# Kernel optimization log

Hardware: AMD Instinct MI355X
Metric: run time of the kernel (lower is better)

The kernel has to match this reference:

```python
import jax, jax.numpy as jnp
import numpy as np

N, E = 50000, 800000
IN_F, HID_F, OUT_F = 128, 128, 32


def setup_inputs() -> dict:
    key = jax.random.key(0)
    ks = jax.random.split(key, 16)
    glorot = lambda k, i, o: jax.random.normal(k, (i, o), jnp.float32) * (2.0 / (i + o)) ** 0.5
    return {
        "x": jax.random.normal(ks[0], (N, IN_F), jnp.float32),
        "src": jax.random.randint(ks[1], (E,), 0, N, jnp.int64),
        "dst": jax.random.randint(ks[2], (E,), 0, N, jnp.int64),
        # layer 0: mean aggregator
        "W_self0": glorot(ks[3], IN_F, HID_F),
        "W_neigh0": glorot(ks[4], IN_F, HID_F),
        "b0": jnp.zeros((HID_F,), jnp.float32),
        # layers 1,2: gcn aggregator (fc_neigh only)
        "W_neigh1": glorot(ks[5], HID_F, HID_F),
        "b1": jnp.zeros((HID_F,), jnp.float32),
        "W_neigh2": glorot(ks[6], HID_F, HID_F),
        "b2": jnp.zeros((HID_F,), jnp.float32),
        # layer 3: mean aggregator
        "W_self3": glorot(ks[7], HID_F, OUT_F),
        "W_neigh3": glorot(ks[8], HID_F, OUT_F),
        "b3": jnp.zeros((OUT_F,), jnp.float32),
    }


def _l2_normalize(x, eps=1e-12):
    # torch F.normalize(x): x / max(||x||_2, eps) along dim 1
    n = jnp.sqrt(jnp.sum(x * x, axis=1, keepdims=True))
    return x / jnp.maximum(n, eps)


def _agg_sum(h, src, dst, n):
    # sum of in-neighbor (src) features onto dst nodes: [N, d]
    return jax.ops.segment_sum(h[src], dst, num_segments=n)


def _sage_mean(h, src, dst, deg, W_self, W_neigh, b):
    nbr = _agg_sum(h, src, dst, h.shape[0]) / jnp.maximum(deg, 1.0)[:, None]
    return h @ W_self + nbr @ W_neigh + b


def _sage_gcn(h, src, dst, deg, W_neigh, b):
    hn = (_agg_sum(h, src, dst, h.shape[0]) + h) / (deg + 1.0)[:, None]
    return hn @ W_neigh + b


def reference(x, src, dst, W_self0, W_neigh0, b0, W_neigh1, b1, W_neigh2, b2,
              W_self3, W_neigh3, b3):
    n = x.shape[0]
    deg = jax.ops.segment_sum(jnp.ones_like(dst, jnp.float32), dst, num_segments=n)
    h = _l2_normalize(x)
    h = jax.nn.relu(_sage_mean(h, src, dst, deg, W_self0, W_neigh0, b0))
    h = jax.nn.relu(_sage_gcn(h, src, dst, deg, W_neigh1, b1))
    h = jax.nn.relu(_sage_gcn(h, src, dst, deg, W_neigh2, b2))
    h = _sage_mean(h, src, dst, deg, W_self3, W_neigh3, b3)  # no relu on last layer
    return h
```

## Files before the change

### kernel.cpp

```cpp
#include <hip/hip_runtime.h>

#define NN 50000
#define NE 800000
#define F  128
#define FO 32

#define RSH  8
#define RSZ  256
#define NBKT 196
#define CAP  5120
#define PCHUNK 4096
#define NPB  ((NE + PCHUNK - 1) / PCHUNK)

typedef _Float16 h16;
typedef h16   half8 __attribute__((ext_vector_type(8)));
typedef h16   h16x2 __attribute__((ext_vector_type(2)));
typedef float f32x4 __attribute__((ext_vector_type(4)));

__global__ __launch_bounds__(256) void k_part(const int* __restrict__ src,
        const int* __restrict__ dst, int* __restrict__ bcur, int* __restrict__ barea) {
    __shared__ int cnt[NBKT];
    __shared__ int base[NBKT];
    const int tid = threadIdx.x;
    const int e0  = blockIdx.x * PCHUNK;
    for (int i = tid; i < NBKT; i += 256) cnt[i] = 0;
    __syncthreads();
    #pragma unroll
    for (int k = 0; k < PCHUNK / 256; ++k) {
        int e = e0 + k * 256 + tid;
        if (e < NE) atomicAdd(&cnt[dst[e] >> RSH], 1);
    }
    __syncthreads();
    for (int i = tid; i < NBKT; i += 256)
        base[i] = atomicAdd(&bcur[i], cnt[i]);
    __syncthreads();
    for (int i = tid; i < NBKT; i += 256) cnt[i] = base[i];
    __syncthreads();
    #pragma unroll
    for (int k = 0; k < PCHUNK / 256; ++k) {
        int e = e0 + k * 256 + tid;
        if (e < NE) {
            int d = dst[e], s = src[e];
            int b = d >> RSH;
            int p = atomicAdd(&cnt[b], 1);
            barea[b * CAP + p] = ((d & (RSZ - 1)) << 16) | s;
        }
    }
}

__global__ __launch_bounds__(256) void k_bscan(const int* __restrict__ bcur,
        int* __restrict__ bpre, int* __restrict__ offs) {
    __shared__ int ws[4];
    const int tid = threadIdx.x, lane = tid & 63, wv = tid >> 6;
    int v = (tid < NBKT) ? bcur[tid] : 0;
    int incl = v;
    #pragma unroll
    for (int d = 1; d < 64; d <<= 1) {
        int t = __shfl_up(incl, d, 64);
        if (lane >= d) incl += t;
    }
    if (lane == 63) ws[wv] = incl;
    __syncthreads();
    if (tid == 0) {
        int run = 0;
        #pragma unroll
        for (int w = 0; w < 4; ++w) { int t = ws[w]; ws[w] = run; run += t; }
    }
    __syncthreads();
    int excl = ws[wv] + incl - v;
    if (tid < NBKT) bpre[tid] = excl;
    if (tid == NBKT - 1) offs[NN] = excl + v;
}

__global__ __launch_bounds__(256) void k_bfill(const int* __restrict__ barea,
        const int* __restrict__ bcur, const int* __restrict__ bpre,
        int* __restrict__ offs, float* __restrict__ degf, int* __restrict__ csr) {
    __shared__ int hist_cur[RSZ];
    __shared__ int ws[4];
    const int r = blockIdx.x, tid = threadIdx.x;
    const int nb    = bcur[r];
    const int gbase = bpre[r];
    const int node  = (r << RSH) + tid;
    hist_cur[tid] = 0;
    __syncthreads();
    const int* area = barea + r * CAP;
    for (int i = tid; i < nb; i += 256) atomicAdd(&hist_cur[area[i] >> 16], 1);
    __syncthreads();
    const int v = hist_cur[tid];
    const int lane = tid & 63, wv = tid >> 6;
    int incl = v;
    #pragma unroll
    for (int d = 1; d < 64; d <<= 1) {
        int t = __shfl_up(incl, d, 64);
        if (lane >= d) incl += t;
    }
    if (lane == 63) ws[wv] = incl;
    __syncthreads();
    if (tid == 0) {
        int run = 0;
        #pragma unroll
        for (int w = 0; w < 4; ++w) { int t = ws[w]; ws[w] = run; run += t; }
    }
    __syncthreads();
    const int ex = ws[wv] + incl - v;
    if (node < NN) {
        offs[node] = gbase + ex;
        degf[node] = (float)v;
    }
    __syncthreads();
    hist_cur[tid] = gbase + ex;
    __syncthreads();
    for (int i = tid; i < nb; i += 256) {
        int pk = area[i];
        int p = atomicAdd(&hist_cur[pk >> 16], 1);
        csr[p] = pk & 0xFFFF;
    }
}

__device__ __forceinline__ void wprep_one(const float* __restrict__ W,
        h16* __restrict__ Wf, int idx, int NC, int NCT) {
    if (idx >= 128 * NC) return;
    int k = idx / NC, n = idx - k * NC;
    int kt = k >> 5, g = (k & 31) >> 3, j = k & 7;
    int ct = n >> 4;
    int lane = g * 16 + (n & 15);
    float w = W[idx];
    h16 hi = (h16)w;
    h16 lo = (h16)(w - (float)hi);
    int base = ((kt * NCT + ct) * 64 + lane) * 8 + j;
    Wf[base] = hi;
    Wf[base + NCT * 2048] = lo;
}

__global__ __launch_bounds__(256) void k_wprep_all(
        const float* __restrict__ S0, const float* __restrict__ N0,
        const float* __restrict__ N1, const float* __restrict__ N2,
        const float* __restrict__ S3, const float* __restrict__ N3,
        h16* fS0, h16* fN0, h16* fN1, h16* fN2, h16* fS3, h16* fN3) {
    int bb = blockIdx.x, tid = threadIdx.x;
    if (bb < 256) {
        const float* W = bb < 64 ? S0 : bb < 128 ? N0 : bb < 192 ? N1 : N2;
        h16*        Wf = bb < 64 ? fS0 : bb < 128 ? fN0 : bb < 192 ? fN1 : fN2;
        wprep_one(W, Wf, (bb & 63) * 256 + tid, 128, 8);
    } else {
        int b2 = bb - 256;
        const float* W = b2 < 16 ? S3 : N3;
        h16*        Wf = b2 < 16 ? fS3 : fN3;
        wprep_one(W, Wf, (b2 & 15) * 256 + tid, 32, 2);
    }
}

__global__ __launch_bounds__(256) void k_l2norm(const float* __restrict__ x,
        h16* __restrict__ hhi, h16* __restrict__ hlo) {
    const int wid  = (int)((blockIdx.x * 256 + threadIdx.x) >> 6);
    const int lane = threadIdx.x & 63;
    if (wid >= NN) return;
    const float2* xr = (const float2*)(x + (size_t)wid * F);
    float2 v = xr[lane];
    float ss = v.x * v.x + v.y * v.y;
    #pragma unroll
    for (int d = 1; d < 64; d <<= 1) ss += __shfl_xor(ss, d, 64);
    float inv = 1.0f / fmaxf(sqrtf(ss), 1e-12f);
    float ox = v.x * inv, oy = v.y * inv;
    h16 hx = (h16)ox, hy = (h16)oy;
    h16x2 vhi = {hx, hy};
    h16x2 vlo = {(h16)(ox - (float)hx), (h16)(oy - (float)hy)};
    *(h16x2*)(hhi + (size_t)wid * F + lane * 2) = vhi;
    *(h16x2*)(hlo + (size_t)wid * F + lane * 2) = vlo;
}

template<int NCT, bool OUT16>
__device__ __forceinline__ void mfma_cols(const half8* Ahi, const half8* Alo,
        const h16* __restrict__ Wf, void* __restrict__ out, int row0, int l) {
    const int cdc = l & 15;
    const int cdr = (l >> 4) * 4;
    #pragma unroll
    for (int ct = 0; ct < NCT; ++ct) {
        f32x4 acc = {0.f, 0.f, 0.f, 0.f};
        #pragma unroll
        for (int kt = 0; kt < 4; ++kt) {
            half8 bh = *(const half8*)(Wf + (size_t)(((kt * NCT + ct) * 64 + l) * 8));
            half8 bl = *(const half8*)(Wf + (size_t)((((4 + kt) * NCT + ct) * 64 + l) * 8));
            acc = __builtin_amdgcn_mfma_f32_16x16x32_f16(Ahi[kt], bh, acc, 0, 0, 0);
            acc = __builtin_amdgcn_mfma_f32_16x16x32_f16(Alo[kt], bh, acc, 0, 0, 0);
            acc = __builtin_amdgcn_mfma_f32_16x16x32_f16(Ahi[kt], bl, acc, 0, 0, 0);
        }
        #pragma unroll
        for (int r = 0; r < 4; ++r) {
            int gr = row0 + cdr + r;
            if (gr < NN) {
                size_t oi = (size_t)gr * (NCT * 16) + ct * 16 + cdc;
                if constexpr (OUT16) ((h16*)out)[oi] = (h16)acc[r];
                else                 ((float*)out)[oi] = acc[r];
            }
        }
    }
}

template<int NCTA, int NCTB, bool A16, bool B16>
__global__ __launch_bounds__(256) void k_mfma(const h16* __restrict__ hhi,
        const h16* __restrict__ hlo, const h16* __restrict__ WfA,
        const h16* __restrict__ WfB, void* __restrict__ outA,
        void* __restrict__ outB) {
    const int tid = threadIdx.x;
    const int l   = tid & 63;
    const int wv  = tid >> 6;
    const int row0 = blockIdx.x * 64 + wv * 16;
    int ar = row0 + (l & 15); if (ar >= NN) ar = NN - 1;
    const size_t ab = (size_t)ar * F + (l >> 4) * 8;
    half8 Ahi[4], Alo[4];
    #pragma unroll
    for (int kt = 0; kt < 4; ++kt) {
        Ahi[kt] = *(const half8*)(hhi + ab + kt * 32);
        Alo[kt] = *(const half8*)(hlo + ab + kt * 32);
    }
    mfma_cols<NCTA, A16>(Ahi, Alo, WfA, outA, row0, l);
    if constexpr (NCTB > 0) mfma_cols<NCTB, B16>(Ahi, Alo, WfB, outB, row0, l);
}

template<int MODE>
__global__ __launch_bounds__(256) void k_agg128(const h16* __restrict__ g,
        const float* __restrict__ s, const int* __restrict__ offs,
        const int* __restrict__ csr, const float* __restrict__ degf,
        const float* __restrict__ b, h16* __restrict__ hhi, h16* __restrict__ hlo) {
    const int wid  = (int)((blockIdx.x * 256 + threadIdx.x) >> 6);
    const int lane = threadIdx.x & 63;
    if (wid >= NN) return;
    const int q  = lane >> 4;
    const int li = lane & 15;
    const int beg = offs[wid], end = offs[wid + 1];
    const half8* g8 = (const half8*)g;
    float a0[8], a1[8];
    #pragma unroll
    for (int j = 0; j < 8; ++j) { a0[j] = 0.f; a1[j] = 0.f; }
    int e = beg;
    for (; e + 16 <= end; e += 16) {
        int u0 = csr[e + q];
        int u1 = csr[e + 4 + q];
        int u2 = csr[e + 8 + q];
        int u3 = csr[e + 12 + q];
        half8 v0 = g8[(size_t)u0 * 16 + li];
        half8 v1 = g8[(size_t)u1 * 16 + li];
        half8 v2 = g8[(size_t)u2 * 16 + li];
        half8 v3 = g8[(size_t)u3 * 16 + li];
        #pragma unroll
        for (int j = 0; j < 8; ++j) {
            a0[j] += (float)v0[j] + (float)v2[j];
            a1[j] += (float)v1[j] + (float)v3[j];
        }
    }
    for (; e + 4 <= end; e += 4) {
        half8 v = g8[(size_t)csr[e + q] * 16 + li];
        #pragma unroll
        for (int j = 0; j < 8; ++j) a0[j] += (float)v[j];
    }
    if (q < end - e) {
        half8 v = g8[(size_t)csr[e + q] * 16 + li];
        #pragma unroll
        for (int j = 0; j < 8; ++j) a1[j] += (float)v[j];
    }
    #pragma unroll
    for (int j = 0; j < 8; ++j) {
        a0[j] += a1[j];
        a0[j] += __shfl_xor(a0[j], 16, 64);
        a0[j] += __shfl_xor(a0[j], 32, 64);
    }
    if (q) return;
    const float dg = degf[wid];
    float bb[8];
    *(float4*)(bb)     = *(const float4*)(b + li * 8);
    *(float4*)(bb + 4) = *(const float4*)(b + li * 8 + 4);
    float r[8];
    if (MODE == 0) {
        float inv = 1.f / fmaxf(dg, 1.f);
        float sv[8];
        *(float4*)(sv)     = *(const float4*)(s + (size_t)wid * F + li * 8);
        *(float4*)(sv + 4) = *(const float4*)(s + (size_t)wid * F + li * 8 + 4);
        #pragma unroll
        for (int j = 0; j < 8; ++j) r[j] = fmaxf(sv[j] + a0[j] * inv + bb[j], 0.f);
    } else {
        float inv = 1.f / (dg + 1.f);
        half8 gv = g8[(size_t)wid * 16 + li];
        #pragma unroll
        for (int j = 0; j < 8; ++j)
            r[j] = fmaxf((a0[j] + (float)gv[j]) * inv + bb[j], 0.f);
    }
    half8 vhi, vlo;
    #pragma unroll
    for (int j = 0; j < 8; ++j) {
        h16 hi = (h16)r[j];
        vhi[j] = hi;
        vlo[j] = (h16)(r[j] - (float)hi);
    }
    *(half8*)(hhi + (size_t)wid * F + li * 8) = vhi;
    *(half8*)(hlo + (size_t)wid * F + li * 8) = vlo;
}

__global__ __launch_bounds__(256) void k_agg32(const float* __restrict__ g,
        const float* __restrict__ s, const int* __restrict__ offs,
        const int* __restrict__ csr, const float* __restrict__ degf,
        const float* __restrict__ b, float* __restrict__ out) {
    const int wid  = (int)((blockIdx.x * 256 + threadIdx.x) >> 6);
    const int lane = threadIdx.x & 63;
    if (wid >= NN) return;
    const int grp = lane >> 3;
    const int li  = lane & 7;
    const int beg = offs[wid], end = offs[wid + 1];
    const float4* g4 = (const float4*)g;
    float4 a0 = make_float4(0, 0, 0, 0), a1 = a0;
    int e = beg + grp;
    for (; e + 8 < end; e += 16) {
        int u0 = csr[e], u1 = csr[e + 8];
        float4 v0 = g4[(size_t)u0 * 8 + li];
        float4 v1 = g4[(size_t)u1 * 8 + li];
        a0.x += v0.x; a0.y += v0.y; a0.z += v0.z; a0.w += v0.w;
        a1.x += v1.x; a1.y += v1.y; a1.z += v1.z; a1.w += v1.w;
    }
    if (e < end) {
        float4 v = g4[(size_t)csr[e] * 8 + li];
        a0.x += v.x; a0.y += v.y; a0.z += v.z; a0.w += v.w;
    }
    a0.x += a1.x; a0.y += a1.y; a0.z += a1.z; a0.w += a1.w;
    #pragma unroll
    for (int d = 8; d < 64; d <<= 1) {
        a0.x += __shfl_xor(a0.x, d, 64);
        a0.y += __shfl_xor(a0.y, d, 64);
        a0.z += __shfl_xor(a0.z, d, 64);
        a0.w += __shfl_xor(a0.w, d, 64);
    }
    if (grp) return;
    const float inv = 1.f / fmaxf(degf[wid], 1.f);
    float4 bb = ((const float4*)b)[li];
    float4 sv = ((const float4*)s)[(size_t)wid * 8 + li];
    float4 r;
    r.x = sv.x + a0.x * inv + bb.x;
    r.y = sv.y + a0.y * inv + bb.y;
    r.z = sv.z + a0.z * inv + bb.z;
    r.w = sv.w + a0.w * inv + bb.w;
    ((float4*)out)[(size_t)wid * 8 + li] = r;
}

extern "C" void kernel_launch(void* const* d_in, const int* in_sizes, int n_in,
                              void* d_out, int out_size, void* d_ws, size_t ws_size,
                              hipStream_t stream) {
    const float* x       = (const float*)d_in[0];
    const int*   src     = (const int*)  d_in[1];
    const int*   dst     = (const int*)  d_in[2];
    const float* Wself0  = (const float*)d_in[3];
    const float* Wneigh0 = (const float*)d_in[4];
    const float* b0      = (const float*)d_in[5];
    const float* Wneigh1 = (const float*)d_in[6];
    const float* b1      = (const float*)d_in[7];
    const float* Wneigh2 = (const float*)d_in[8];
    const float* b2      = (const float*)d_in[9];
    const float* Wself3  = (const float*)d_in[10];
    const float* Wneigh3 = (const float*)d_in[11];
    const float* b3      = (const float*)d_in[12];
    float* out = (float*)d_out;

    char* ws = (char*)d_ws;
    size_t off = 0;
    auto alloc = [&](size_t bytes) -> void* {
        void* p = ws + off;
        off += (bytes + 255) & ~(size_t)255;
        return p;
    };
    float* degf   = (float*)alloc((size_t)NN * 4);
    int*   offs   = (int*)  alloc((size_t)(NN + 1) * 4);
    int*   csr    = (int*)  alloc((size_t)NE * 4);
    int*   bcur   = (int*)  alloc((size_t)NBKT * 4);
    int*   bpre   = (int*)  alloc((size_t)NBKT * 4);
    int*   barea  = (int*)  alloc((size_t)NBKT * CAP * 4);
    h16*   hhi    = (h16*)  alloc((size_t)NN * F * 2);
    h16*   hlo    = (h16*)  alloc((size_t)NN * F * 2);
    h16*   gh     = (h16*)  alloc((size_t)NN * F * 2);
    float* bufg   = (float*)alloc((size_t)NN * F * 4);
    float* bufs   = (float*)alloc((size_t)NN * F * 4);
    h16*   WfS0   = (h16*)  alloc((size_t)128 * 128 * 2 * 2);
    h16*   WfN0   = (h16*)  alloc((size_t)128 * 128 * 2 * 2);
    h16*   WfN1   = (h16*)  alloc((size_t)128 * 128 * 2 * 2);
    h16*   WfN2   = (h16*)  alloc((size_t)128 * 128 * 2 * 2);
    h16*   WfS3   = (h16*)  alloc((size_t)128 * 32 * 2 * 2);
    h16*   WfN3   = (h16*)  alloc((size_t)128 * 32 * 2 * 2);

    hipMemsetAsync(bcur, 0, (size_t)NBKT * 4, stream);

    const int wgrid = (NN + 3) / 4;
    const int mgrid = (NN + 63) / 64;

    k_wprep_all<<<288, 256, 0, stream>>>(Wself0, Wneigh0, Wneigh1, Wneigh2,
                                         Wself3, Wneigh3,
                                         WfS0, WfN0, WfN1, WfN2, WfS3, WfN3);

    k_part  <<<NPB, 256, 0, stream>>>(src, dst, bcur, barea);
    k_bscan <<<1, 256, 0, stream>>>(bcur, bpre, offs);
    k_bfill <<<NBKT, 256, 0, stream>>>(barea, bcur, bpre, offs, degf, csr);
    k_l2norm<<<wgrid, 256, 0, stream>>>(x, hhi, hlo);

    k_mfma<8, 8, false, true><<<mgrid, 256, 0, stream>>>(hhi, hlo, WfS0, WfN0, bufs, gh);
    k_agg128<0><<<wgrid, 256, 0, stream>>>(gh, bufs, offs, csr, degf, b0, hhi, hlo);

    k_mfma<8, 0, true, false><<<mgrid, 256, 0, stream>>>(hhi, hlo, WfN1, nullptr, gh, nullptr);
    k_agg128<1><<<wgrid, 256, 0, stream>>>(gh, nullptr, offs, csr, degf, b1, hhi, hlo);

    k_mfma<8, 0, true, false><<<mgrid, 256, 0, stream>>>(hhi, hlo, WfN2, nullptr, gh, nullptr);
    k_agg128<1><<<wgrid, 256, 0, stream>>>(gh, nullptr, offs, csr, degf, b2, hhi, hlo);

    k_mfma<2, 2, false, false><<<mgrid, 256, 0, stream>>>(hhi, hlo, WfS3, WfN3, bufs, bufg);
    k_agg32<<<wgrid, 256, 0, stream>>>(bufg, bufs, offs, csr, degf, b3, out);
}
```

Baseline: 325.0 us.

## Merge preprocessing kernels and store self/neighbor projections in fp16

Folds the memset, bucket scan and l2norm into combined launches (k_pre0 zeroes the bucket counters, k_pre1 runs partitioning and normalization side by side, k_bfill recomputes the bucket prefix per block). The layer-0 self term and the layer-3 self and neighbor projections are now written and read as fp16 instead of fp32, which halves the bytes moved in those aggregations. This cuts launch count and memory traffic, at the cost of lower precision in intermediates that were fp32 before and a small amount of redundant scan work in every bfill block.

```diff
diff --git a/kernel.cpp b/kernel.cpp
--- a/kernel.cpp
+++ b/kernel.cpp
@@ -11,111 +11,13 @@
 #define CAP  5120
 #define PCHUNK 4096
 #define NPB  ((NE + PCHUNK - 1) / PCHUNK)
+#define LGRID ((NN + 3) / 4)
 
 typedef _Float16 h16;
 typedef h16   half8 __attribute__((ext_vector_type(8)));
+typedef h16   h16x4 __attribute__((ext_vector_type(4)));
 typedef h16   h16x2 __attribute__((ext_vector_type(2)));
 typedef float f32x4 __attribute__((ext_vector_type(4)));
-
-__global__ __launch_bounds__(256) void k_part(const int* __restrict__ src,
-        const int* __restrict__ dst, int* __restrict__ bcur, int* __restrict__ barea) {
-    __shared__ int cnt[NBKT];
-    __shared__ int base[NBKT];
-    const int tid = threadIdx.x;
-    const int e0  = blockIdx.x * PCHUNK;
-    for (int i = tid; i < NBKT; i += 256) cnt[i] = 0;
-    __syncthreads();
-    #pragma unroll
-    for (int k = 0; k < PCHUNK / 256; ++k) {
-        int e = e0 + k * 256 + tid;
-        if (e < NE) atomicAdd(&cnt[dst[e] >> RSH], 1);
-    }
-    __syncthreads();
-    for (int i = tid; i < NBKT; i += 256)
-        base[i] = atomicAdd(&bcur[i], cnt[i]);
-    __syncthreads();
-    for (int i = tid; i < NBKT; i += 256) cnt[i] = base[i];
-    __syncthreads();
-    #pragma unroll
-    for (int k = 0; k < PCHUNK / 256; ++k) {
-        int e = e0 + k * 256 + tid;
-        if (e < NE) {
-            int d = dst[e], s = src[e];
-            int b = d >> RSH;
-            int p = atomicAdd(&cnt[b], 1);
-            barea[b * CAP + p] = ((d & (RSZ - 1)) << 16) | s;
-        }
-    }
-}
-
-__global__ __launch_bounds__(256) void k_bscan(const int* __restrict__ bcur,
-        int* __restrict__ bpre, int* __restrict__ offs) {
-    __shared__ int ws[4];
-    const int tid = threadIdx.x, lane = tid & 63, wv = tid >> 6;
-    int v = (tid < NBKT) ? bcur[tid] : 0;
-    int incl = v;
-    #pragma unroll
-    for (int d = 1; d < 64; d <<= 1) {
-        int t = __shfl_up(incl, d, 64);
-        if (lane >= d) incl += t;
-    }
-    if (lane == 63) ws[wv] = incl;
-    __syncthreads();
-    if (tid == 0) {
-        int run = 0;
-        #pragma unroll
-        for (int w = 0; w < 4; ++w) { int t = ws[w]; ws[w] = run; run += t; }
-    }
-    __syncthreads();
-    int excl = ws[wv] + incl - v;
-    if (tid < NBKT) bpre[tid] = excl;
-    if (tid == NBKT - 1) offs[NN] = excl + v;
-}
-
-__global__ __launch_bounds__(256) void k_bfill(const int* __restrict__ barea,
-        const int* __restrict__ bcur, const int* __restrict__ bpre,
-        int* __restrict__ offs, float* __restrict__ degf, int* __restrict__ csr) {
-    __shared__ int hist_cur[RSZ];
-    __shared__ int ws[4];
-    const int r = blockIdx.x, tid = threadIdx.x;
-    const int nb    = bcur[r];
-    const int gbase = bpre[r];
-    const int node  = (r << RSH) + tid;
-    hist_cur[tid] = 0;
-    __syncthreads();
-    const int* area = barea + r * CAP;
-    for (int i = tid; i < nb; i += 256) atomicAdd(&hist_cur[area[i] >> 16], 1);
-    __syncthreads();
-    const int v = hist_cur[tid];
-    const int lane = tid & 63, wv = tid >> 6;
-    int incl = v;
-    #pragma unroll
-    for (int d = 1; d < 64; d <<= 1) {
-        int t = __shfl_up(incl, d, 64);
-        if (lane >= d) incl += t;
-    }
-    if (lane == 63) ws[wv] = incl;
-    __syncthreads();
-    if (tid == 0) {
-        int run = 0;
-        #pragma unroll
-        for (int w = 0; w < 4; ++w) { int t = ws[w]; ws[w] = run; run += t; }
-    }
-    __syncthreads();
-    const int ex = ws[wv] + incl - v;
-    if (node < NN) {
-        offs[node] = gbase + ex;
-        degf[node] = (float)v;
-    }
-    __syncthreads();
-    hist_cur[tid] = gbase + ex;
-    __syncthreads();
-    for (int i = tid; i < nb; i += 256) {
-        int pk = area[i];
-        int p = atomicAdd(&hist_cur[pk >> 16], 1);
-        csr[p] = pk & 0xFFFF;
-    }
-}
 
 __device__ __forceinline__ void wprep_one(const float* __restrict__ W,
         h16* __restrict__ Wf, int idx, int NC, int NCT) {
@@ -132,41 +34,141 @@
     Wf[base + NCT * 2048] = lo;
 }
 
-__global__ __launch_bounds__(256) void k_wprep_all(
+__global__ __launch_bounds__(256) void k_pre0(
         const float* __restrict__ S0, const float* __restrict__ N0,
         const float* __restrict__ N1, const float* __restrict__ N2,
         const float* __restrict__ S3, const float* __restrict__ N3,
-        h16* fS0, h16* fN0, h16* fN1, h16* fN2, h16* fS3, h16* fN3) {
+        h16* fS0, h16* fN0, h16* fN1, h16* fN2, h16* fS3, h16* fN3,
+        int* __restrict__ bcur) {
     int bb = blockIdx.x, tid = threadIdx.x;
     if (bb < 256) {
         const float* W = bb < 64 ? S0 : bb < 128 ? N0 : bb < 192 ? N1 : N2;
         h16*        Wf = bb < 64 ? fS0 : bb < 128 ? fN0 : bb < 192 ? fN1 : fN2;
         wprep_one(W, Wf, (bb & 63) * 256 + tid, 128, 8);
-    } else {
+    } else if (bb < 288) {
         int b2 = bb - 256;
         const float* W = b2 < 16 ? S3 : N3;
         h16*        Wf = b2 < 16 ? fS3 : fN3;
         wprep_one(W, Wf, (b2 & 15) * 256 + tid, 32, 2);
-    }
-}
-
-__global__ __launch_bounds__(256) void k_l2norm(const float* __restrict__ x,
-        h16* __restrict__ hhi, h16* __restrict__ hlo) {
-    const int wid  = (int)((blockIdx.x * 256 + threadIdx.x) >> 6);
-    const int lane = threadIdx.x & 63;
-    if (wid >= NN) return;
-    const float2* xr = (const float2*)(x + (size_t)wid * F);
-    float2 v = xr[lane];
-    float ss = v.x * v.x + v.y * v.y;
-    #pragma unroll
-    for (int d = 1; d < 64; d <<= 1) ss += __shfl_xor(ss, d, 64);
-    float inv = 1.0f / fmaxf(sqrtf(ss), 1e-12f);
-    float ox = v.x * inv, oy = v.y * inv;
-    h16 hx = (h16)ox, hy = (h16)oy;
-    h16x2 vhi = {hx, hy};
-    h16x2 vlo = {(h16)(ox - (float)hx), (h16)(oy - (float)hy)};
-    *(h16x2*)(hhi + (size_t)wid * F + lane * 2) = vhi;
-    *(h16x2*)(hlo + (size_t)wid * F + lane * 2) = vlo;
+    } else {
+        if (tid < NBKT) bcur[tid] = 0;
+    }
+}
+
+__global__ __launch_bounds__(256) void k_pre1(const int* __restrict__ src,
+        const int* __restrict__ dst, int* __restrict__ bcur, int* __restrict__ barea,
+        const float* __restrict__ x, h16* __restrict__ hhi, h16* __restrict__ hlo) {
+    __shared__ int cnt[NBKT];
+    __shared__ int base[NBKT];
+    const int tid = threadIdx.x;
+    if ((int)blockIdx.x < NPB) {
+        const int e0 = blockIdx.x * PCHUNK;
+        for (int i = tid; i < NBKT; i += 256) cnt[i] = 0;
+        __syncthreads();
+        #pragma unroll
+        for (int k = 0; k < PCHUNK / 256; ++k) {
+            int e = e0 + k * 256 + tid;
+            if (e < NE) atomicAdd(&cnt[dst[e] >> RSH], 1);
+        }
+        __syncthreads();
+        for (int i = tid; i < NBKT; i += 256)
+            base[i] = atomicAdd(&bcur[i], cnt[i]);
+        __syncthreads();
+        for (int i = tid; i < NBKT; i += 256) cnt[i] = base[i];
+        __syncthreads();
+        #pragma unroll
+        for (int k = 0; k < PCHUNK / 256; ++k) {
+            int e = e0 + k * 256 + tid;
+            if (e < NE) {
+                int d = dst[e], s = src[e];
+                int b = d >> RSH;
+                int p = atomicAdd(&cnt[b], 1);
+                barea[b * CAP + p] = ((d & (RSZ - 1)) << 16) | s;
+            }
+        }
+    } else {
+        const int bb   = blockIdx.x - NPB;
+        const int wid  = bb * 4 + (tid >> 6);
+        const int lane = tid & 63;
+        if (wid >= NN) return;
+        const float2* xr = (const float2*)(x + (size_t)wid * F);
+        float2 v = xr[lane];
+        float ss = v.x * v.x + v.y * v.y;
+        #pragma unroll
+        for (int d = 1; d < 64; d <<= 1) ss += __shfl_xor(ss, d, 64);
+        float inv = 1.0f / fmaxf(sqrtf(ss), 1e-12f);
+        float ox = v.x * inv, oy = v.y * inv;
+        h16 hx = (h16)ox, hy = (h16)oy;
+        h16x2 vhi = {hx, hy};
+        h16x2 vlo = {(h16)(ox - (float)hx), (h16)(oy - (float)hy)};
+        *(h16x2*)(hhi + (size_t)wid * F + lane * 2) = vhi;
+        *(h16x2*)(hlo + (size_t)wid * F + lane * 2) = vlo;
+    }
+}
+
+__global__ __launch_bounds__(256) void k_bfill(const int* __restrict__ barea,
+        const int* __restrict__ bcur, int* __restrict__ offs,
+        float* __restrict__ degf, int* __restrict__ csr) {
+    __shared__ int pre[NBKT];
+    __shared__ int hist_cur[RSZ];
+    __shared__ int ws[4];
+    const int r = blockIdx.x, tid = threadIdx.x;
+    const int lane = tid & 63, wv = tid >> 6;
+    int bv = (tid < NBKT) ? bcur[tid] : 0;
+    int bi = bv;
+    #pragma unroll
+    for (int d = 1; d < 64; d <<= 1) {
+        int t = __shfl_up(bi, d, 64);
+        if (lane >= d) bi += t;
+    }
+    if (lane == 63) ws[wv] = bi;
+    __syncthreads();
+    if (tid == 0) {
+        int run = 0;
+        #pragma unroll
+        for (int w = 0; w < 4; ++w) { int t = ws[w]; ws[w] = run; run += t; }
+    }
+    __syncthreads();
+    if (tid < NBKT) pre[tid] = ws[wv] + bi - bv;
+    if (r == 0 && tid == NBKT - 1) offs[NN] = ws[wv] + bi;
+    __syncthreads();
+    const int nb    = bcur[r];
+    const int gbase = pre[r];
+    const int node  = (r << RSH) + tid;
+    hist_cur[tid] = 0;
+    __syncthreads();
+    const int* area = barea + r * CAP;
+    for (int i = tid; i < nb; i += 256) atomicAdd(&hist_cur[area[i] >> 16], 1);
+    __syncthreads();
+    const int v = hist_cur[tid];
+    int incl = v;
+    #pragma unroll
+    for (int d = 1; d < 64; d <<= 1) {
+        int t = __shfl_up(incl, d, 64);
+        if (lane >= d) incl += t;
+    }
+    __syncthreads();
+    if (lane == 63) ws[wv] = incl;
+    __syncthreads();
+    if (tid == 0) {
+        int run = 0;
+        #pragma unroll
+        for (int w = 0; w < 4; ++w) { int t = ws[w]; ws[w] = run; run += t; }
+    }
+    __syncthreads();
+    const int ex = ws[wv] + incl - v;
+    if (node < NN) {
+        offs[node] = gbase + ex;
+        degf[node] = (float)v;
+    }
+    __syncthreads();
+    hist_cur[tid] = gbase + ex;
+    __syncthreads();
+    for (int i = tid; i < nb; i += 256) {
+        int pk = area[i];
+        int p = atomicAdd(&hist_cur[pk >> 16], 1);
+        csr[p] = pk & 0xFFFF;
+    }
 }
 
 template<int NCT, bool OUT16>
@@ -220,7 +222,7 @@
 
 template<int MODE>
 __global__ __launch_bounds__(256) void k_agg128(const h16* __restrict__ g,
-        const float* __restrict__ s, const int* __restrict__ offs,
+        const h16* __restrict__ s, const int* __restrict__ offs,
         const int* __restrict__ csr, const float* __restrict__ degf,
         const float* __restrict__ b, h16* __restrict__ hhi, h16* __restrict__ hlo) {
     const int wid  = (int)((blockIdx.x * 256 + threadIdx.x) >> 6);
@@ -273,11 +275,10 @@
     float r[8];
     if (MODE == 0) {
         float inv = 1.f / fmaxf(dg, 1.f);
-        float sv[8];
-        *(float4*)(sv)     = *(const float4*)(s + (size_t)wid * F + li * 8);
-        *(float4*)(sv + 4) = *(const float4*)(s + (size_t)wid * F + li * 8 + 4);
-        #pragma unroll
-        for (int j = 0; j < 8; ++j) r[j] = fmaxf(sv[j] + a0[j] * inv + bb[j], 0.f);
+        half8 sv = ((const half8*)s)[(size_t)wid * 16 + li];
+        #pragma unroll
+        for (int j = 0; j < 8; ++j)
+            r[j] = fmaxf((float)sv[j] + a0[j] * inv + bb[j], 0.f);
     } else {
         float inv = 1.f / (dg + 1.f);
         half8 gv = g8[(size_t)wid * 16 + li];
@@ -296,8 +297,8 @@
     *(half8*)(hlo + (size_t)wid * F + li * 8) = vlo;
 }
 
-__global__ __launch_bounds__(256) void k_agg32(const float* __restrict__ g,
-        const float* __restrict__ s, const int* __restrict__ offs,
+__global__ __launch_bounds__(256) void k_agg32(const h16* __restrict__ g,
+        const h16* __restrict__ s, const int* __restrict__ offs,
         const int* __restrict__ csr, const float* __restrict__ degf,
         const float* __restrict__ b, float* __restrict__ out) {
     const int wid  = (int)((blockIdx.x * 256 + threadIdx.x) >> 6);
@@ -306,37 +307,37 @@
     const int grp = lane >> 3;
     const int li  = lane & 7;
     const int beg = offs[wid], end = offs[wid + 1];
-    const float4* g4 = (const float4*)g;
-    float4 a0 = make_float4(0, 0, 0, 0), a1 = a0;
+    const h16x4* g4 = (const h16x4*)g;
+    float a0[4] = {0.f, 0.f, 0.f, 0.f}, a1[4] = {0.f, 0.f, 0.f, 0.f};
     int e = beg + grp;
     for (; e + 8 < end; e += 16) {
         int u0 = csr[e], u1 = csr[e + 8];
-        float4 v0 = g4[(size_t)u0 * 8 + li];
-        float4 v1 = g4[(size_t)u1 * 8 + li];
-        a0.x += v0.x; a0.y += v0.y; a0.z += v0.z; a0.w += v0.w;
-        a1.x += v1.x; a1.y += v1.y; a1.z += v1.z; a1.w += v1.w;
+        h16x4 v0 = g4[(size_t)u0 * 8 + li];
+        h16x4 v1 = g4[(size_t)u1 * 8 + li];
+        #pragma unroll
+        for (int j = 0; j < 4; ++j) { a0[j] += (float)v0[j]; a1[j] += (float)v1[j]; }
     }
     if (e < end) {
-        float4 v = g4[(size_t)csr[e] * 8 + li];
-        a0.x += v.x; a0.y += v.y; a0.z += v.z; a0.w += v.w;
-    }
-    a0.x += a1.x; a0.y += a1.y; a0.z += a1.z; a0.w += a1.w;
-    #pragma unroll
-    for (int d = 8; d < 64; d <<= 1) {
-        a0.x += __shfl_xor(a0.x, d, 64);
-        a0.y += __shfl_xor(a0.y, d, 64);
-        a0.z += __shfl_xor(a0.z, d, 64);
-        a0.w += __shfl_xor(a0.w, d, 64);
+        h16x4 v = g4[(size_t)csr[e] * 8 + li];
+        #pragma unroll
+        for (int j = 0; j < 4; ++j) a0[j] += (float)v[j];
+    }
+    #pragma unroll
+    for (int j = 0; j < 4; ++j) {
+        a0[j] += a1[j];
+        a0[j] += __shfl_xor(a0[j], 8, 64);
+        a0[j] += __shfl_xor(a0[j], 16, 64);
+        a0[j] += __shfl_xor(a0[j], 32, 64);
     }
     if (grp) return;
     const float inv = 1.f / fmaxf(degf[wid], 1.f);
     float4 bb = ((const float4*)b)[li];
-    float4 sv = ((const float4*)s)[(size_t)wid * 8 + li];
+    h16x4 sv = ((const h16x4*)s)[(size_t)wid * 8 + li];
     float4 r;
-    r.x = sv.x + a0.x * inv + bb.x;
-    r.y = sv.y + a0.y * inv + bb.y;
-    r.z = sv.z + a0.z * inv + bb.z;
-    r.w = sv.w + a0.w * inv + bb.w;
+    r.x = (float)sv[0] + a0[0] * inv + bb.x;
+    r.y = (float)sv[1] + a0[1] * inv + bb.y;
+    r.z = (float)sv[2] + a0[2] * inv + bb.z;
+    r.w = (float)sv[3] + a0[3] * inv + bb.w;
     ((float4*)out)[(size_t)wid * 8 + li] = r;
 }
 
@@ -369,13 +370,11 @@
     int*   offs   = (int*)  alloc((size_t)(NN + 1) * 4);
     int*   csr    = (int*)  alloc((size_t)NE * 4);
     int*   bcur   = (int*)  alloc((size_t)NBKT * 4);
-    int*   bpre   = (int*)  alloc((size_t)NBKT * 4);
     int*   barea  = (int*)  alloc((size_t)NBKT * CAP * 4);
     h16*   hhi    = (h16*)  alloc((size_t)NN * F * 2);
     h16*   hlo    = (h16*)  alloc((size_t)NN * F * 2);
     h16*   gh     = (h16*)  alloc((size_t)NN * F * 2);
-    float* bufg   = (float*)alloc((size_t)NN * F * 4);
-    float* bufs   = (float*)alloc((size_t)NN * F * 4);
+    h16*   s16    = (h16*)  alloc((size_t)NN * F * 2);
     h16*   WfS0   = (h16*)  alloc((size_t)128 * 128 * 2 * 2);
     h16*   WfN0   = (h16*)  alloc((size_t)128 * 128 * 2 * 2);
     h16*   WfN1   = (h16*)  alloc((size_t)128 * 128 * 2 * 2);
@@ -383,29 +382,23 @@
     h16*   WfS3   = (h16*)  alloc((size_t)128 * 32 * 2 * 2);
     h16*   WfN3   = (h16*)  alloc((size_t)128 * 32 * 2 * 2);
 
-    hipMemsetAsync(bcur, 0, (size_t)NBKT * 4, stream);
-
-    const int wgrid = (NN + 3) / 4;
     const int mgrid = (NN + 63) / 64;
 
-    k_wprep_all<<<288, 256, 0, stream>>>(Wself0, Wneigh0, Wneigh1, Wneigh2,
-                                         Wself3, Wneigh3,
-                                         WfS0, WfN0, WfN1, WfN2, WfS3, WfN3);
-
-    k_part  <<<NPB, 256, 0, stream>>>(src, dst, bcur, barea);
-    k_bscan <<<1, 256, 0, stream>>>(bcur, bpre, offs);
-    k_bfill <<<NBKT, 256, 0, stream>>>(barea, bcur, bpre, offs, degf, csr);
-    k_l2norm<<<wgrid, 256, 0, stream>>>(x, hhi, hlo);
-
-    k_mfma<8, 8, false, true><<<mgrid, 256, 0, stream>>>(hhi, hlo, WfS0, WfN0, bufs, gh);
-    k_agg128<0><<<wgrid, 256, 0, stream>>>(gh, bufs, offs, csr, degf, b0, hhi, hlo);
+    k_pre0<<<289, 256, 0, stream>>>(Wself0, Wneigh0, Wneigh1, Wneigh2,
+                                    Wself3, Wneigh3,
+                                    WfS0, WfN0, WfN1, WfN2, WfS3, WfN3, bcur);
+    k_pre1<<<NPB + LGRID, 256, 0, stream>>>(src, dst, bcur, barea, x, hhi, hlo);
+    k_bfill<<<NBKT, 256, 0, stream>>>(barea, bcur, offs, degf, csr);
+
+    k_mfma<8, 8, true, true><<<mgrid, 256, 0, stream>>>(hhi, hlo, WfS0, WfN0, s16, gh);
+    k_agg128<0><<<LGRID, 256, 0, stream>>>(gh, s16, offs, csr, degf, b0, hhi, hlo);
 
     k_mfma<8, 0, true, false><<<mgrid, 256, 0, stream>>>(hhi, hlo, WfN1, nullptr, gh, nullptr);
-    k_agg128<1><<<wgrid, 256, 0, stream>>>(gh, nullptr, offs, csr, degf, b1, hhi, hlo);
+    k_agg128<1><<<LGRID, 256, 0, stream>>>(gh, nullptr, offs, csr, degf, b1, hhi, hlo);
 
     k_mfma<8, 0, true, false><<<mgrid, 256, 0, stream>>>(hhi, hlo, WfN2, nullptr, gh, nullptr);
-    k_agg128<1><<<wgrid, 256, 0, stream>>>(gh, nullptr, offs, csr, degf, b2, hhi, hlo);
-
-    k_mfma<2, 2, false, false><<<mgrid, 256, 0, stream>>>(hhi, hlo, WfS3, WfN3, bufs, bufg);
-    k_agg32<<<wgrid, 256, 0, stream>>>(bufg, bufs, offs, csr, degf, b3, out);
-}
+    k_agg128<1><<<LGRID, 256, 0, stream>>>(gh, nullptr, offs, csr, degf, b2, hhi, hlo);
+
+    k_mfma<2, 2, true, true><<<mgrid, 256, 0, stream>>>(hhi, hlo, WfS3, WfN3, s16, gh);
+    k_agg32<<<LGRID, 256, 0, stream>>>(gh, s16, offs, csr, degf, b3, out);
+}
```

After: 313.7 us. 1.04x faster.
